# Kernel optimization log

Hardware: AMD Instinct MI355X
Metric: run time of the kernel (lower is better)

## Reference

```python
import jax, jax.numpy as jnp
import numpy as np

INPUT_SIZE = 128
OUTPUT_SIZE = 32
LIFTING_DIM = 512
BATCH = 32768


def setup_inputs() -> dict:
    key = jax.random.key(0)
    ks = jax.random.split(key, 7)
    x = jax.random.normal(ks[0], (BATCH, INPUT_SIZE), dtype=jnp.float32)
    # Linear(input_size, lifting_dim) with bias (torch layout: W [out, in])
    lim1 = 1.0 / np.sqrt(INPUT_SIZE)
    W1 = jax.random.uniform(ks[1], (LIFTING_DIM, INPUT_SIZE), jnp.float32, -lim1, lim1)
    b1 = jax.random.uniform(ks[2], (LIFTING_DIM,), jnp.float32, -lim1, lim1)
    # Linear(lifting_dim, output_size, bias=False)
    lim2 = 1.0 / np.sqrt(LIFTING_DIM)
    W2 = jax.random.uniform(ks[3], (OUTPUT_SIZE, LIFTING_DIM), jnp.float32, -lim2, lim2)
    # Quadratic params: L_vars ~ randn, b ~ randn, c ~ randn (as in module init)
    n_tril = LIFTING_DIM * (LIFTING_DIM + 1) // 2
    L_vars = jax.random.normal(ks[4], (n_tril,), dtype=jnp.float32)
    qb = jax.random.normal(ks[5], (LIFTING_DIM,), dtype=jnp.float32)
    qc = jax.random.normal(ks[6], (1,), dtype=jnp.float32)
    return {"x": x, "W1": W1, "b1": b1, "W2": W2, "L_vars": L_vars, "qb": qb, "qc": qc}


def reference(x, W1, b1, W2, L_vars, qb, qc):
    # lifting: phi = tanh(x @ W1^T + b1)   [B, lifting_dim]
    phi = jnp.tanh(x @ W1.T + b1)
    # actor: linear feedback (no bias)     [B, output_size]
    pi = phi @ W2.T
    # critic: quadratic form y = phi' Q phi + b' phi + c with Q = L L^T (PSD)
    rows, cols = jnp.tril_indices(LIFTING_DIM)  # row-major, same order as torch.tril_indices
    L = jnp.zeros((LIFTING_DIM, LIFTING_DIM), dtype=L_vars.dtype).at[rows, cols].set(L_vars)
    Q = L @ L.T
    # diag(phi @ Q @ phi.T) == sum((phi @ Q) * phi, axis=1)  -- O(B*d^2), same math
    y = jnp.sum((phi @ Q) * phi, axis=1) + phi @ qb + qc  # [B]
    vf = y[:, None]  # [B, 1]
    return pi, vf
```

## Files before the change

### kernel.cpp

```cpp
#include <hip/hip_runtime.h>
#include <hip/hip_bf16.h>
#include <stdint.h>

typedef short bf16x8 __attribute__((ext_vector_type(8)));
typedef float f32x4 __attribute__((ext_vector_type(4)));

#define DEVI static __device__ __forceinline__

constexpr int B_   = 32768;
constexpr int IN_  = 128;
constexpr int LF_  = 512;
constexpr int OUT_ = 32;

constexpr size_t OFF_LTF = 0;
constexpr size_t OFF_W1F = 524288;
constexpr size_t OFF_W2F = OFF_W1F + 131072;

DEVI short f2bs(float f) { __hip_bfloat16 h = __float2bfloat16(f); return *(short*)&h; }

DEVI float tanh_fast(float v) {
    float e = __expf(2.0f * v);
    return 1.0f - 2.0f * __builtin_amdgcn_rcpf(e + 1.0f);
}

DEVI bf16x8 fragGL(const __hip_bfloat16* base, int chunk, int ln) {
    return *(const bf16x8*)(base + ((size_t)chunk * 64 + ln) * 8);
}

DEVI bf16x8 phiFrag(const char* p, int row, int kofs) {
    int c = (kofs >> 3) ^ (row & 7);
    return *(const bf16x8*)(p + (size_t)((row << 6) + c) * 16);
}
DEVI void phiStore(char* p, int row, int col, float v) {
    int c = (col >> 3) ^ (row & 7);
    *(short*)(p + (size_t)((row << 6) + c) * 16 + (col & 7) * 2) = f2bs(v);
}
DEVI bf16x8 xFrag(const char* p, int row, int kofs) {
    int c = (kofs >> 3) ^ (row & 15);
    return *(const bf16x8*)(p + (size_t)((row << 4) + c) * 16);
}

__global__ __launch_bounds__(256) void k_prep(
        const float* __restrict__ w1, const float* __restrict__ w2,
        const float* __restrict__ lv, const float* __restrict__ qb,
        __hip_bfloat16* __restrict__ w1f, __hip_bfloat16* __restrict__ w2f,
        __hip_bfloat16* __restrict__ ltf) {
    int cid = blockIdx.x * 256 + threadIdx.x;
    if (cid < 8192) {
        int ln = cid & 63, ks = (cid >> 6) & 3, nt = cid >> 8;
        int n = nt * 16 + (ln & 15), kb = ks * 32 + (ln >> 4) * 8;
        const float* src = w1 + (size_t)n * IN_ + kb;
        bf16x8 o;
#pragma unroll
        for (int i = 0; i < 8; ++i) o[i] = f2bs(src[i]);
        *(bf16x8*)(w1f + (size_t)cid * 8) = o;
    } else if (cid < 11264) {
        int c2 = cid - 8192;
        int ln = c2 & 63, ks = (c2 >> 6) & 15, nt = c2 >> 10;
        int n = nt * 16 + (ln & 15), kb = ks * 32 + (ln >> 4) * 8;
        bf16x8 o;
#pragma unroll
        for (int i = 0; i < 8; ++i) {
            float v = (n < OUT_) ? w2[(size_t)n * LF_ + kb + i]
                                 : (n == OUT_ ? qb[kb + i] : 0.f);
            o[i] = f2bs(v);
        }
        *(bf16x8*)(w2f + (size_t)c2 * 8) = o;
    } else if (cid < 44032) {
        int c3 = cid - 11264;
        int ln = c3 & 63, ks = (c3 >> 6) & 15, t = c3 >> 10;
        int j = t * 16 + (ln & 15), kb = ks * 32 + (ln >> 4) * 8;
        bf16x8 o;
#pragma unroll
        for (int i = 0; i < 8; ++i) {
            int k = kb + i;
            o[i] = (k >= j) ? f2bs(lv[(size_t)k * (k + 1) / 2 + j]) : (short)0;
        }
        *(bf16x8*)(ltf + (size_t)c3 * 8) = o;
    }
}

__global__ __launch_bounds__(512, 4) void k_fused(
        const float* __restrict__ x, const __hip_bfloat16* __restrict__ w1f,
        const float* __restrict__ b1, const __hip_bfloat16* __restrict__ w2f,
        const __hip_bfloat16* __restrict__ ltf, const float* __restrict__ qcp,
        float* __restrict__ pi, float* __restrict__ vf) {
    __shared__ char smem[81920];
    char*  phiB  = smem;
    char*  stage = smem + 65536;
    float* vfb   = (float*)stage;
    float* vfp   = (float*)(stage + 256);

    const int tid = threadIdx.x, wv = tid >> 6, ln = tid & 63;
    const int cl = ln & 15, q = ln >> 4;
    const int m0 = blockIdx.x * 64;

#pragma unroll
    for (int it = 0; it < 2; ++it) {
        int slot = it * 512 + tid, row = slot >> 4, cg = slot & 15;
        const float4* p = (const float4*)(x + (size_t)(m0 + row) * IN_ + cg * 8);
        float4 u0 = p[0], u1 = p[1];
        bf16x8 pk;
        pk[0] = f2bs(u0.x); pk[1] = f2bs(u0.y); pk[2] = f2bs(u0.z); pk[3] = f2bs(u0.w);
        pk[4] = f2bs(u1.x); pk[5] = f2bs(u1.y); pk[6] = f2bs(u1.z); pk[7] = f2bs(u1.w);
        *(bf16x8*)(stage + (size_t)((row << 4) + (cg ^ (row & 15))) * 16) = pk;
    }
    __syncthreads();

    {
        f32x4 acc[4][4] = {};
#pragma unroll
        for (int ks = 0; ks < 4; ++ks) {
            bf16x8 a[4], bfr[4];
#pragma unroll
            for (int mi = 0; mi < 4; ++mi) a[mi] = xFrag(stage, mi * 16 + cl, ks * 32 + q * 8);
#pragma unroll
            for (int ni = 0; ni < 4; ++ni)
                bfr[ni] = fragGL(w1f, (4 * wv + ni) * 4 + ks, ln);
#pragma unroll
            for (int mi = 0; mi < 4; ++mi)
#pragma unroll
                for (int ni = 0; ni < 4; ++ni)
                    acc[mi][ni] = __builtin_amdgcn_mfma_f32_16x16x32_bf16(
                        a[mi], bfr[ni], acc[mi][ni], 0, 0, 0);
        }
#pragma unroll
        for (int ni = 0; ni < 4; ++ni) {
            int colg = wv * 64 + ni * 16 + cl;
            float bv = b1[colg];
#pragma unroll
            for (int mi = 0; mi < 4; ++mi)
#pragma unroll
                for (int r = 0; r < 4; ++r)
                    phiStore(phiB, mi * 16 + q * 4 + r, colg,
                             tanh_fast(acc[mi][ni][r] + bv));
        }
    }
    __syncthreads();

    {
        int ids[2] = { (wv < 4) ? 2 * wv : 8 + (wv - 4), (wv < 4) ? 2 * wv + 1 : -1 };
#pragma unroll
        for (int u = 0; u < 2; ++u) {
            int id = ids[u];
            if (id < 0) continue;
            int mi = id & 3, ni = id >> 2;
            f32x4 a2 = {};
            for (int ks = 0; ks < 16; ++ks) {
                bf16x8 a = phiFrag(phiB, mi * 16 + cl, ks * 32 + q * 8);
                bf16x8 b = fragGL(w2f, ni * 16 + ks, ln);
                a2 = __builtin_amdgcn_mfma_f32_16x16x32_bf16(a, b, a2, 0, 0, 0);
            }
#pragma unroll
            for (int r = 0; r < 4; ++r) {
                int row = mi * 16 + q * 4 + r, col = ni * 16 + cl;
                if (col < OUT_)       pi[(size_t)(m0 + row) * OUT_ + col] = a2[r];
                else if (col == OUT_) vfb[row] = a2[r];
            }
        }
    }

    {
        int tl[4] = { wv, 15 - wv, 16 + wv, 31 - wv };
        int kstart[4];
#pragma unroll
        for (int j = 0; j < 4; ++j) kstart[j] = (tl[j] * 16) & ~31;
        int kmin = min(min(kstart[0], kstart[1]), min(kstart[2], kstart[3]));
        f32x4 acc[4][4] = {};
        for (int k0 = kmin; k0 < LF_; k0 += 32) {
            int ks = k0 >> 5;
            bf16x8 a[4];
#pragma unroll
            for (int mi = 0; mi < 4; ++mi) a[mi] = phiFrag(phiB, mi * 16 + cl, k0 + q * 8);
#pragma unroll
            for (int j = 0; j < 4; ++j) {
                if (k0 >= kstart[j]) {
                    bf16x8 b = fragGL(ltf, tl[j] * 16 + ks, ln);
#pragma unroll
                    for (int mi = 0; mi < 4; ++mi)
                        acc[j][mi] = __builtin_amdgcn_mfma_f32_16x16x32_bf16(
                            a[mi], b, acc[j][mi], 0, 0, 0);
                }
            }
        }
        float vacc[4][4];
#pragma unroll
        for (int mi = 0; mi < 4; ++mi)
#pragma unroll
            for (int r = 0; r < 4; ++r) {
                float s = 0.f;
#pragma unroll
                for (int j = 0; j < 4; ++j) { float t = acc[j][mi][r]; s += t * t; }
                s += __shfl_xor(s, 1, 64);
                s += __shfl_xor(s, 2, 64);
                s += __shfl_xor(s, 4, 64);
                s += __shfl_xor(s, 8, 64);
                vacc[mi][r] = s;
            }
        if (cl == 0)
#pragma unroll
            for (int mi = 0; mi < 4; ++mi)
#pragma unroll
                for (int r = 0; r < 4; ++r)
                    vfp[wv * 64 + mi * 16 + q * 4 + r] = vacc[mi][r];
    }
    __syncthreads();
    if (tid < 64) {
        float v = vfb[tid] + qcp[0];
#pragma unroll
        for (int w = 0; w < 8; ++w) v += vfp[w * 64 + tid];
        vf[m0 + tid] = v;
    }
}

extern "C" void kernel_launch(void* const* d_in, const int* in_sizes, int n_in,
                              void* d_out, int out_size, void* d_ws, size_t ws_size,
                              hipStream_t stream) {
    const float* x  = (const float*)d_in[0];
    const float* w1 = (const float*)d_in[1];
    const float* b1 = (const float*)d_in[2];
    const float* w2 = (const float*)d_in[3];
    const float* lv = (const float*)d_in[4];
    const float* qb = (const float*)d_in[5];
    const float* qc = (const float*)d_in[6];

    char* ws = (char*)d_ws;
    __hip_bfloat16* ltf = (__hip_bfloat16*)(ws + OFF_LTF);
    __hip_bfloat16* w1f = (__hip_bfloat16*)(ws + OFF_W1F);
    __hip_bfloat16* w2f = (__hip_bfloat16*)(ws + OFF_W2F);

    float* pi = (float*)d_out;
    float* vf = pi + (size_t)B_ * OUT_;

    k_prep <<<172, 256, 0, stream>>>(w1, w2, lv, qb, w1f, w2f, ltf);
    k_fused<<<B_ / 64, 512, 0, stream>>>(x, w1f, b1, w2f, ltf, qc, pi, vf);
}
```

Before: 105.3 us.

## Prefetch weight fragments, transpose first GEMM for packed phi stores

The first GEMM swaps its MFMA operands so each lane holds four consecutive phi columns. The tanh outputs can then be written to shared memory as packed 8-byte stores instead of single shorts, and the bias is loaded as a float4. Global weight fragments for W1 and the L-tile loop are software-prefetched one k-step ahead, and the W2 loop is fully unrolled. This is meant to hide global load latency and cut LDS store count, at the cost of more live registers under the launch bound of 4 waves.

```diff
diff --git a/kernel.cpp b/kernel.cpp
--- a/kernel.cpp
+++ b/kernel.cpp
@@ -30,10 +30,6 @@
 DEVI bf16x8 phiFrag(const char* p, int row, int kofs) {
     int c = (kofs >> 3) ^ (row & 7);
     return *(const bf16x8*)(p + (size_t)((row << 6) + c) * 16);
-}
-DEVI void phiStore(char* p, int row, int col, float v) {
-    int c = (col >> 3) ^ (row & 7);
-    *(short*)(p + (size_t)((row << 6) + c) * 16 + (col & 7) * 2) = f2bs(v);
 }
 DEVI bf16x8 xFrag(const char* p, int row, int kofs) {
     int c = (kofs >> 3) ^ (row & 15);
@@ -109,31 +105,42 @@
 
     {
         f32x4 acc[4][4] = {};
+        bf16x8 wfr[4], wnx[4];
+#pragma unroll
+        for (int ni = 0; ni < 4; ++ni) wfr[ni] = fragGL(w1f, (4 * wv + ni) * 4, ln);
 #pragma unroll
         for (int ks = 0; ks < 4; ++ks) {
-            bf16x8 a[4], bfr[4];
+            bf16x8 a[4];
 #pragma unroll
             for (int mi = 0; mi < 4; ++mi) a[mi] = xFrag(stage, mi * 16 + cl, ks * 32 + q * 8);
+            if (ks < 3)
+#pragma unroll
+                for (int ni = 0; ni < 4; ++ni)
+                    wnx[ni] = fragGL(w1f, (4 * wv + ni) * 4 + ks + 1, ln);
 #pragma unroll
             for (int ni = 0; ni < 4; ++ni)
-                bfr[ni] = fragGL(w1f, (4 * wv + ni) * 4 + ks, ln);
-#pragma unroll
-            for (int mi = 0; mi < 4; ++mi)
-#pragma unroll
-                for (int ni = 0; ni < 4; ++ni)
-                    acc[mi][ni] = __builtin_amdgcn_mfma_f32_16x16x32_bf16(
-                        a[mi], bfr[ni], acc[mi][ni], 0, 0, 0);
+#pragma unroll
+                for (int mi = 0; mi < 4; ++mi)
+                    acc[ni][mi] = __builtin_amdgcn_mfma_f32_16x16x32_bf16(
+                        wfr[ni], a[mi], acc[ni][mi], 0, 0, 0);
+#pragma unroll
+            for (int ni = 0; ni < 4; ++ni) wfr[ni] = wnx[ni];
         }
 #pragma unroll
         for (int ni = 0; ni < 4; ++ni) {
-            int colg = wv * 64 + ni * 16 + cl;
-            float bv = b1[colg];
-#pragma unroll
-            for (int mi = 0; mi < 4; ++mi)
-#pragma unroll
-                for (int r = 0; r < 4; ++r)
-                    phiStore(phiB, mi * 16 + q * 4 + r, colg,
-                             tanh_fast(acc[mi][ni][r] + bv));
+            float4 bb = *(const float4*)(b1 + wv * 64 + ni * 16 + q * 4);
+            int c0 = wv * 8 + ni * 2 + (q >> 1);
+#pragma unroll
+            for (int mi = 0; mi < 4; ++mi) {
+                int row = mi * 16 + cl;
+                short4 pk;
+                pk.x = f2bs(tanh_fast(acc[ni][mi][0] + bb.x));
+                pk.y = f2bs(tanh_fast(acc[ni][mi][1] + bb.y));
+                pk.z = f2bs(tanh_fast(acc[ni][mi][2] + bb.z));
+                pk.w = f2bs(tanh_fast(acc[ni][mi][3] + bb.w));
+                *(short4*)(phiB + (size_t)((row << 6) + (c0 ^ (row & 7))) * 16
+                           + (q & 1) * 8) = pk;
+            }
         }
     }
     __syncthreads();
@@ -146,6 +153,7 @@
             if (id < 0) continue;
             int mi = id & 3, ni = id >> 2;
             f32x4 a2 = {};
+#pragma unroll
             for (int ks = 0; ks < 16; ++ks) {
                 bf16x8 a = phiFrag(phiB, mi * 16 + cl, ks * 32 + q * 8);
                 bf16x8 b = fragGL(w2f, ni * 16 + ks, ln);
@@ -161,29 +169,40 @@
     }
 
     {
-        int tl[4] = { wv, 15 - wv, 16 + wv, 31 - wv };
+        const int tl[4] = { wv, 15 - wv, 16 + wv, 31 - wv };
         int kstart[4];
 #pragma unroll
         for (int j = 0; j < 4; ++j) kstart[j] = (tl[j] * 16) & ~31;
-        int kmin = min(min(kstart[0], kstart[1]), min(kstart[2], kstart[3]));
+        const int kmin = kstart[0];
         f32x4 acc[4][4] = {};
+        bf16x8 b[4];
+#pragma unroll
+        for (int j = 0; j < 4; ++j)
+            if (kmin >= kstart[j]) b[j] = fragGL(ltf, tl[j] * 16 + (kmin >> 5), ln);
         for (int k0 = kmin; k0 < LF_; k0 += 32) {
-            int ks = k0 >> 5;
+            int k1 = k0 + 32;
             bf16x8 a[4];
 #pragma unroll
             for (int mi = 0; mi < 4; ++mi) a[mi] = phiFrag(phiB, mi * 16 + cl, k0 + q * 8);
+            bf16x8 bn[4];
+            if (k1 < LF_) {
+                int ks1 = k1 >> 5;
+#pragma unroll
+                for (int j = 0; j < 4; ++j)
+                    if (k1 >= kstart[j]) bn[j] = fragGL(ltf, tl[j] * 16 + ks1, ln);
+            }
 #pragma unroll
             for (int j = 0; j < 4; ++j) {
                 if (k0 >= kstart[j]) {
-                    bf16x8 b = fragGL(ltf, tl[j] * 16 + ks, ln);
 #pragma unroll
                     for (int mi = 0; mi < 4; ++mi)
                         acc[j][mi] = __builtin_amdgcn_mfma_f32_16x16x32_bf16(
-                            a[mi], b, acc[j][mi], 0, 0, 0);
+                            a[mi], b[j], acc[j][mi], 0, 0, 0);
                 }
             }
-        }
-        float vacc[4][4];
+#pragma unroll
+            for (int j = 0; j < 4; ++j) b[j] = bn[j];
+        }
 #pragma unroll
         for (int mi = 0; mi < 4; ++mi)
 #pragma unroll
@@ -195,14 +214,8 @@
                 s += __shfl_xor(s, 2, 64);
                 s += __shfl_xor(s, 4, 64);
                 s += __shfl_xor(s, 8, 64);
-                vacc[mi][r] = s;
-            }
-        if (cl == 0)
-#pragma unroll
-            for (int mi = 0; mi < 4; ++mi)
-#pragma unroll
-                for (int r = 0; r < 4; ++r)
-                    vfp[wv * 64 + mi * 16 + q * 4 + r] = vacc[mi][r];
+                if (cl == 0) vfp[wv * 64 + mi * 16 + q * 4 + r] = s;
+            }
     }
     __syncthreads();
     if (tid < 64) {
```

Result: slower. 108.6 us (+3.1%).
